# Kernel optimization log

Hardware: AMD Instinct MI355X
Metric: run time of the kernel (lower is better)

The kernel has to match this reference:

```python
import jax, jax.numpy as jnp
import numpy as np

N_NODES = 100000
N_EDGES = 1600000
N_GRAPHS = 128
ATOM_F = 92
BOND_F = 41
EMB = 64
HID = 128
CHG = 16
N_LAYERS = 3
EPS = 1e-5


def setup_inputs() -> dict:
    key = jax.random.key(0)
    ks = jax.random.split(key, 32)
    s = 0.05
    inp = {
        "x": jax.random.normal(ks[0], (N_NODES, ATOM_F), jnp.float32),
        "edge_attr": jax.random.uniform(ks[1], (N_EDGES, BOND_F), jnp.float32),
        "charge": jax.random.normal(ks[2], (N_GRAPHS,), jnp.float32),
        "edge_index": jax.random.randint(ks[3], (2, N_EDGES), 0, N_NODES),
        "batch": jnp.sort(jax.random.randint(ks[4], (N_NODES,), 0, N_GRAPHS)),
        # embeddings
        "W_charge": jax.random.normal(ks[5], (1, CHG), jnp.float32) * s,
        "b_charge": jnp.zeros((CHG,), jnp.float32),
        "W_atom": jax.random.normal(ks[6], (ATOM_F + CHG, EMB), jnp.float32) * s,
        "b_atom": jnp.zeros((EMB,), jnp.float32),
        "W_bond": jax.random.normal(ks[7], (BOND_F, EMB), jnp.float32) * s,
        "b_bond": jnp.zeros((EMB,), jnp.float32),
        # conv layers (stacked over layer dim)
        "conv_eW1": jax.random.normal(ks[8], (N_LAYERS, 3 * EMB, EMB), jnp.float32) * s,
        "conv_eb1": jnp.zeros((N_LAYERS, EMB), jnp.float32),
        "conv_eW2": jax.random.normal(ks[9], (N_LAYERS, EMB, EMB), jnp.float32) * s,
        "conv_eb2": jnp.zeros((N_LAYERS, EMB), jnp.float32),
        "conv_nW1": jax.random.normal(ks[10], (N_LAYERS, 2 * EMB, EMB), jnp.float32) * s,
        "conv_nb1": jnp.zeros((N_LAYERS, EMB), jnp.float32),
        "conv_nW2": jax.random.normal(ks[11], (N_LAYERS, EMB, EMB), jnp.float32) * s,
        "conv_nb2": jnp.zeros((N_LAYERS, EMB), jnp.float32),
        "bn_gamma": jnp.ones((N_LAYERS, EMB), jnp.float32),
        "bn_beta": jnp.zeros((N_LAYERS, EMB), jnp.float32),
        # predictor
        "pW1": jax.random.normal(ks[12], (EMB, HID), jnp.float32) * s,
        "pb1": jnp.zeros((HID,), jnp.float32),
        "pW2": jax.random.normal(ks[13], (HID, HID), jnp.float32) * s,
        "pb2": jnp.zeros((HID,), jnp.float32),
        "pW3": jax.random.normal(ks[14], (HID, 1), jnp.float32) * s,
        "pb3": jnp.zeros((1,), jnp.float32),
    }
    return inp


def reference(x, edge_attr, charge, W_charge, b_charge, W_atom, b_atom,
              W_bond, b_bond, conv_eW1, conv_eb1, conv_eW2, conv_eb2,
              conv_nW1, conv_nb1, conv_nW2, conv_nb2, bn_gamma, bn_beta,
              pW1, pb1, pW2, pb2, pW3, pb3, edge_index, batch):
    sp = jax.nn.softplus
    n_nodes = x.shape[0]
    n_graphs = charge.shape[0]

    # early charge integration: per-graph charge embedding broadcast to nodes
    charge_feat = charge[:, None] @ W_charge + b_charge          # [B, CHG]
    x = jnp.concatenate([x, charge_feat[batch]], axis=1)          # [N, ATOM_F+CHG]
    x = x @ W_atom + b_atom                                       # [N, EMB]
    ea = edge_attr @ W_bond + b_bond                              # [E, EMB]

    row, col = edge_index[0], edge_index[1]
    for i in range(conv_eW1.shape[0]):
        xr, xc = x[row], x[col]                                   # gathers [E, EMB]
        # edge update: MLP on [x_row, x_col, edge_attr]
        e_in = jnp.concatenate([xr, xc, ea], axis=1)              # [E, 3*EMB]
        ea = sp(e_in @ conv_eW1[i] + conv_eb1[i]) @ conv_eW2[i] + conv_eb2[i]
        # node messages: MLP on [x_row, new edge_attr]
        m_in = jnp.concatenate([xr, ea], axis=1)                  # [E, 2*EMB]
        msg = sp(m_in @ conv_nW1[i] + conv_nb1[i]) @ conv_nW2[i] + conv_nb2[i]
        x_new = jax.ops.segment_sum(msg, col, num_segments=n_nodes)
        # BatchNorm1d (training-mode batch stats, biased variance)
        mean = jnp.mean(x_new, axis=0)
        var = jnp.var(x_new, axis=0)
        x_new = (x_new - mean) * jax.lax.rsqrt(var + EPS) * bn_gamma[i] + bn_beta[i]
        x = sp(x_new) + x                                         # residual

    # global mean pool over graphs
    sums = jax.ops.segment_sum(x, batch, num_segments=n_graphs)   # [B, EMB]
    cnt = jax.ops.segment_sum(jnp.ones((n_nodes, 1), x.dtype), batch, num_segments=n_graphs)
    g = sums / jnp.maximum(cnt, 1.0)

    # predictor MLP (dropout is identity in eval mode)
    h = sp(g @ pW1 + pb1)
    h = sp(h @ pW2 + pb2)
    out = h @ pW3 + pb3                                           # [B, 1]
    return out.squeeze(-1)
```

## Files before the change

### kernel.cpp

```cpp
#include <hip/hip_runtime.h>
#include <math.h>

typedef short v8s __attribute__((ext_vector_type(8)));
typedef float v4f __attribute__((ext_vector_type(4)));
typedef unsigned int u32x4 __attribute__((ext_vector_type(4)));

__device__ __forceinline__ u32x4 nt_load4(const void* p) {
  return __builtin_nontemporal_load((const u32x4*)p);
}
__device__ __forceinline__ void nt_store4(void* p, u32x4 v) {
  __builtin_nontemporal_store(v, (u32x4*)p);
}

__device__ __forceinline__ float sp_f(float x) {
  return fmaxf(x, 0.0f) + 0.69314718056f * __log2f(1.0f + __expf(-fabsf(x)));
}

__device__ __forceinline__ unsigned short f2bf(float f) {
  union { float f; unsigned u; } x; x.f = f;
  unsigned r = (x.u + 0x7FFF + ((x.u >> 16) & 1)) >> 16;
  return (unsigned short)r;
}

__device__ __forceinline__ float bf2f(unsigned short h) {
  union { unsigned u; float f; } x; x.u = ((unsigned)h) << 16;
  return x.f;
}

__global__ __launch_bounds__(256) void k_prep_wfrag(
    const float* __restrict__ eW1, const float* __restrict__ eW2,
    const float* __restrict__ nW1, const float* __restrict__ nW2,
    const float* __restrict__ W_bond, unsigned short* __restrict__ wfrag) {
  if (blockIdx.x == 12) {
    unsigned short* out = wfrag + 12 * 4096;
    for (int f = threadIdx.x; f < 4096; f += 256) {
      int j = f & 7, ln = (f >> 3) & 63, kh = (f >> 9) & 1, ct = f >> 10;
      int k = kh * 32 + (ln >> 4) * 8 + j;
      int n = ct * 16 + (ln & 15);
      out[f] = (k < 41) ? f2bf(W_bond[k * 64 + n]) : 0;
    }
    return;
  }
  int i = blockIdx.x >> 2;
  int m = blockIdx.x & 3;
  const float* W;
  if (m == 0)      W = eW1 + (size_t)i * 192 * 64 + 128 * 64;
  else if (m == 1) W = eW2 + (size_t)i * 64 * 64;
  else if (m == 2) W = nW1 + (size_t)i * 128 * 64 + 64 * 64;
  else             W = nW2 + (size_t)i * 64 * 64;
  unsigned short* out = wfrag + ((size_t)i * 4 + m) * 4096;
  for (int f = threadIdx.x; f < 4096; f += 256) {
    int j = f & 7, ln = (f >> 3) & 63, kh = (f >> 9) & 1, ct = f >> 10;
    int k = kh * 32 + (ln >> 4) * 8 + j;
    int n = ct * 16 + (ln & 15);
    out[f] = f2bf(W[k * 64 + n]);
  }
}

__global__ __launch_bounds__(256) void k_embed_nodes(
    const float* __restrict__ x, const int* __restrict__ batch,
    const float* __restrict__ charge, const float* __restrict__ W_charge,
    const float* __restrict__ b_charge, const float* __restrict__ W_atom,
    const float* __restrict__ b_atom, float* __restrict__ xemb, int N) {
  __shared__ float sW[108 * 64];
  __shared__ float sX[128 * 92];
  __shared__ float sb[64];
  __shared__ float sWc[16];
  __shared__ float sbc[16];
  for (int i = threadIdx.x; i < 108 * 64; i += blockDim.x) sW[i] = W_atom[i];
  if (threadIdx.x < 64) sb[threadIdx.x] = b_atom[threadIdx.x];
  if (threadIdx.x < 16) {
    sWc[threadIdx.x] = W_charge[threadIdx.x];
    sbc[threadIdx.x] = b_charge[threadIdx.x];
  }
  int ntiles = (N + 127) >> 7;
  for (int tile = blockIdx.x; tile < ntiles; tile += gridDim.x) {
    int base = tile << 7;
    int cnt = N - base; if (cnt > 128) cnt = 128;
    __syncthreads();
    if (cnt == 128) {
      const u32x4* src = (const u32x4*)(x + (size_t)base * 92);
      for (int i = threadIdx.x; i < 2944; i += 256)
        ((u32x4*)sX)[i] = nt_load4(&src[i]);
    } else {
      for (int i = threadIdx.x; i < cnt * 92; i += 256)
        sX[i] = x[(size_t)base * 92 + i];
    }
    __syncthreads();
    int t = threadIdx.x;
    int node = t & 127, half = t >> 7;
    if (node < cnt) {
      int n = base + node;
      float acc[32];
#pragma unroll
      for (int j = 0; j < 32; ++j) acc[j] = sb[half * 32 + j];
      const float* xr = sX + node * 92;
      for (int k = 0; k < 92; ++k) {
        float a = xr[k];
        const float* wk = sW + k * 64 + half * 32;
#pragma unroll
        for (int j = 0; j < 32; ++j) acc[j] = fmaf(a, wk[j], acc[j]);
      }
      float ch = charge[batch[n]];
#pragma unroll
      for (int c = 0; c < 16; ++c) {
        float cf = fmaf(ch, sWc[c], sbc[c]);
        const float* wk = sW + (92 + c) * 64 + half * 32;
#pragma unroll
        for (int j = 0; j < 32; ++j) acc[j] = fmaf(cf, wk[j], acc[j]);
      }
      float* o = xemb + (size_t)n * 64 + half * 32;
#pragma unroll
      for (int q8 = 0; q8 < 8; ++q8)
        ((float4*)o)[q8] = make_float4(acc[4*q8], acc[4*q8+1], acc[4*q8+2], acc[4*q8+3]);
    }
  }
}

__global__ __launch_bounds__(256) void k_hist(const int* __restrict__ col,
                                              int* __restrict__ counts, int E) {
  int stride = gridDim.x * blockDim.x;
  for (int e = blockIdx.x * blockDim.x + threadIdx.x; e < E; e += stride)
    atomicAdd(&counts[col[e]], 1);
}

__global__ __launch_bounds__(256) void k_scan1(const int* __restrict__ counts,
                                               int* __restrict__ scan_tmp,
                                               int* __restrict__ bsum, int N) {
  __shared__ int sd[2][256];
  int t = threadIdx.x;
  int i = blockIdx.x * 256 + t;
  int v = (i < N) ? counts[i] : 0;
  sd[0][t] = v;
  __syncthreads();
  int s = 0;
#pragma unroll
  for (int off = 1; off < 256; off <<= 1) {
    int nv = sd[s][t];
    if (t >= off) nv += sd[s][t - off];
    sd[s ^ 1][t] = nv;
    s ^= 1;
    __syncthreads();
  }
  if (i < N) scan_tmp[i] = sd[s][t];
  if (t == 255) bsum[blockIdx.x] = sd[s][255];
}

__global__ __launch_bounds__(256) void k_scan2(int* __restrict__ b, int NB) {
  __shared__ int sd[2][256];
  __shared__ int carry_s;
  int t = threadIdx.x;
  if (t == 0) carry_s = 0;
  __syncthreads();
  for (int base = 0; base < NB; base += 256) {
    int i = base + t;
    int v = (i < NB) ? b[i] : 0;
    sd[0][t] = v;
    __syncthreads();
    int s = 0;
#pragma unroll
    for (int off = 1; off < 256; off <<= 1) {
      int nv = sd[s][t];
      if (t >= off) nv += sd[s][t - off];
      sd[s ^ 1][t] = nv;
      s ^= 1;
      __syncthreads();
    }
    int c = carry_s;
    int tot = sd[s][255];
    if (i < NB) b[i] = sd[s][t] + c;
    __syncthreads();
    if (t == 0) carry_s = c + tot;
    __syncthreads();
  }
}

__global__ __launch_bounds__(256) void k_scan3(const int* __restrict__ counts,
                                               const int* __restrict__ scan_tmp,
                                               const int* __restrict__ bsum,
                                               int* __restrict__ cursor, int N) {
  int i = blockIdx.x * 256 + threadIdx.x;
  if (i < N) {
    int base = (blockIdx.x > 0) ? bsum[blockIdx.x - 1] : 0;
    cursor[i] = scan_tmp[i] - counts[i] + base;
  }
}

__global__ __launch_bounds__(256) void k_scatter(
    const int* __restrict__ row, const int* __restrict__ col,
    int* __restrict__ cursor, int* __restrict__ pos,
    int* __restrict__ row_s, int* __restrict__ col_s, int E) {
  int stride = gridDim.x * blockDim.x;
  for (int e = blockIdx.x * blockDim.x + threadIdx.x; e < E; e += stride) {
    int c = col[e];
    int p = atomicAdd(&cursor[c], 1);
    pos[e] = p;
    row_s[p] = row[e];
    col_s[p] = c;
  }
}

__global__ __launch_bounds__(256) void k_embed_bonds_mfma(
    const float* __restrict__ eattr, const int* __restrict__ pos,
    const unsigned short* __restrict__ gWb, const float* __restrict__ b_bond,
    unsigned short* __restrict__ ea16, int E) {
  __shared__ unsigned short sA[128 * 64];
  __shared__ float sb[64];
  __shared__ int spos[128];
  int tid = threadIdx.x;
  int w = tid >> 6, l = tid & 63, q = l >> 4, c16 = l & 15;
  int rbase = w * 32;
  if (tid < 64) sb[tid] = b_bond[tid];
  int ntiles = (E + 127) >> 7;
  for (int tile = blockIdx.x; tile < ntiles; tile += gridDim.x) {
    int te = tile << 7;
    int cnt = E - te; if (cnt > 128) cnt = 128;
    __syncthreads();
    uint4 z = make_uint4(0, 0, 0, 0);
    for (int i = tid; i < 1024; i += 256) ((uint4*)sA)[i] = z;
    __syncthreads();
    int nflt = cnt * 41;
    for (int i = tid; i < nflt; i += 256) {
      int r = i / 41, k = i - r * 41;
      float v = __builtin_nontemporal_load(&eattr[(size_t)te * 41 + i]);
      sA[r * 64 + (k ^ ((r & 7) << 3))] = f2bf(v);
    }
    if (tid < 128) spos[tid] = (te + tid < E) ? pos[te + tid] : -1;
    __syncthreads();
    v8s bfr[4][2], af[2][2];
    v4f acc[2][4];
    const v8s* wp_ = (const v8s*)gWb;
#pragma unroll
    for (int ct = 0; ct < 4; ++ct)
#pragma unroll
      for (int kh = 0; kh < 2; ++kh)
        bfr[ct][kh] = wp_[(ct * 2 + kh) * 64 + l];
#pragma unroll
    for (int rb = 0; rb < 2; ++rb)
#pragma unroll
      for (int kh = 0; kh < 2; ++kh) {
        int row_ = rbase + rb * 16 + c16;
        af[rb][kh] = *(const v8s*)&sA[row_ * 64 +
                                      ((kh * 32 + q * 8) ^ ((row_ & 7) << 3))];
      }
#pragma unroll
    for (int rb = 0; rb < 2; ++rb)
#pragma unroll
      for (int ct = 0; ct < 4; ++ct) {
        v4f a_ = {0.f, 0.f, 0.f, 0.f};
        a_ = __builtin_amdgcn_mfma_f32_16x16x32_bf16(af[rb][0], bfr[ct][0], a_, 0, 0, 0);
        a_ = __builtin_amdgcn_mfma_f32_16x16x32_bf16(af[rb][1], bfr[ct][1], a_, 0, 0, 0);
        acc[rb][ct] = a_;
      }
#pragma unroll
    for (int rb = 0; rb < 2; ++rb)
#pragma unroll
      for (int ct = 0; ct < 4; ++ct) {
        int n = ct * 16 + c16;
#pragma unroll
        for (int r = 0; r < 4; ++r) {
          float v = acc[rb][ct][r] + sb[n];
          int row = rbase + rb * 16 + q * 4 + r;
          sA[row * 64 + (n ^ ((row & 7) << 3))] = f2bf(v);
        }
      }
    __syncthreads();
    for (int i = tid; i < 1024; i += 256) {
      int r = i >> 3, cc = i & 7;
      int p = spos[r];
      if (p >= 0) {
        u32x4 d = *(const u32x4*)&sA[r * 64 + ((cc * 8) ^ ((r & 7) << 3))];
        nt_store4(&ea16[(size_t)p * 64 + cc * 8], d);
      }
    }
  }
}

__device__ __forceinline__ void node_pre_body(
    const float* __restrict__ xr, const float* sWa, const float* sWb,
    const float* sWp, unsigned short* __restrict__ up16,
    unsigned short* __restrict__ v16, int n) {
  const float4* xr4 = (const float4*)xr;
  float u[64], p[64];
#pragma unroll
  for (int j = 0; j < 64; ++j) { u[j] = 0.f; p[j] = 0.f; }
  for (int k4 = 0; k4 < 16; ++k4) {
    float4 av = xr4[k4];
    const float* wa = sWa + k4 * 256;
    const float* wp = sWp + k4 * 256;
#pragma unroll
    for (int j = 0; j < 64; ++j) u[j] = fmaf(av.x, wa[j], u[j]);
#pragma unroll
    for (int j = 0; j < 64; ++j) p[j] = fmaf(av.x, wp[j], p[j]);
#pragma unroll
    for (int j = 0; j < 64; ++j) u[j] = fmaf(av.y, wa[64 + j], u[j]);
#pragma unroll
    for (int j = 0; j < 64; ++j) p[j] = fmaf(av.y, wp[64 + j], p[j]);
#pragma unroll
    for (int j = 0; j < 64; ++j) u[j] = fmaf(av.z, wa[128 + j], u[j]);
#pragma unroll
    for (int j = 0; j < 64; ++j) p[j] = fmaf(av.z, wp[128 + j], p[j]);
#pragma unroll
    for (int j = 0; j < 64; ++j) u[j] = fmaf(av.w, wa[192 + j], u[j]);
#pragma unroll
    for (int j = 0; j < 64; ++j) p[j] = fmaf(av.w, wp[192 + j], p[j]);
  }
  unsigned short* o = up16 + (size_t)n * 128;
#pragma unroll
  for (int q8 = 0; q8 < 8; ++q8) {
    unsigned short tmp[8];
#pragma unroll
    for (int j = 0; j < 8; ++j) {
      int i = q8 * 8 + j;
      tmp[j] = f2bf(u[((i & 3) << 4) | (i >> 2)]);
    }
    *(uint4*)&o[q8 * 8] = *(uint4*)tmp;
  }
#pragma unroll
  for (int q8 = 0; q8 < 8; ++q8) {
    unsigned short tmp[8];
#pragma unroll
    for (int j = 0; j < 8; ++j) {
      int i = q8 * 8 + j;
      tmp[j] = f2bf(p[((i & 3) << 4) | (i >> 2)]);
    }
    *(uint4*)&o[64 + q8 * 8] = *(uint4*)tmp;
  }
  float vv[64];
#pragma unroll
  for (int j = 0; j < 64; ++j) vv[j] = 0.f;
  for (int k4 = 0; k4 < 16; ++k4) {
    float4 av = xr4[k4];
    const float* wb = sWb + k4 * 256;
#pragma unroll
    for (int j = 0; j < 64; ++j) vv[j] = fmaf(av.x, wb[j], vv[j]);
#pragma unroll
    for (int j = 0; j < 64; ++j) vv[j] = fmaf(av.y, wb[64 + j], vv[j]);
#pragma unroll
    for (int j = 0; j < 64; ++j) vv[j] = fmaf(av.z, wb[128 + j], vv[j]);
#pragma unroll
    for (int j = 0; j < 64; ++j) vv[j] = fmaf(av.w, wb[192 + j], vv[j]);
  }
  unsigned short* ov = v16 + (size_t)n * 64;
#pragma unroll
  for (int q8 = 0; q8 < 8; ++q8) {
    unsigned short tmp[8];
#pragma unroll
    for (int j = 0; j < 8; ++j) {
      int i = q8 * 8 + j;
      tmp[j] = f2bf(vv[((i & 3) << 4) | (i >> 2)]);
    }
    *(uint4*)&ov[q8 * 8] = *(uint4*)tmp;
  }
}

__global__ __launch_bounds__(256) void k_node_pre(
    const float* __restrict__ xemb, const float* __restrict__ eW1,
    const float* __restrict__ nW1, unsigned short* __restrict__ up16,
    unsigned short* __restrict__ v16, float* __restrict__ xnew, int N) {
  __shared__ float sWa[64 * 64];
  __shared__ float sWb[64 * 64];
  __shared__ float sWp[64 * 64];
  for (int i = threadIdx.x; i < 64 * 64; i += blockDim.x) {
    sWa[i] = eW1[i];
    sWb[i] = eW1[64 * 64 + i];
    sWp[i] = nW1[i];
  }
  __syncthreads();
  int stride = gridDim.x * blockDim.x;
  float4 z = make_float4(0.f, 0.f, 0.f, 0.f);
  for (int n = blockIdx.x * blockDim.x + threadIdx.x; n < N; n += stride) {
    node_pre_body(xemb + (size_t)n * 64, sWa, sWb, sWp, up16, v16, n);
    float4* xz = (float4*)(xnew + (size_t)n * 64);
#pragma unroll
    for (int q = 0; q < 16; ++q) xz[q] = z;
  }
}

__global__ __launch_bounds__(256) void k_bn_pre(
    float* __restrict__ xemb, float* __restrict__ xnew,
    const float* __restrict__ bnacc, const float* __restrict__ gamma,
    const float* __restrict__ beta, const float* __restrict__ eW1n,
    const float* __restrict__ nW1n, unsigned short* __restrict__ up16,
    unsigned short* __restrict__ v16, int N) {
  __shared__ float sWa[64 * 64];
  __shared__ float sWb[64 * 64];
  __shared__ float sWp[64 * 64];
  __shared__ float sscale[64], sshift[64];
  for (int i = threadIdx.x; i < 64 * 64; i += blockDim.x) {
    sWa[i] = eW1n[i];
    sWb[i] = eW1n[64 * 64 + i];
    sWp[i] = nW1n[i];
  }
  if (threadIdx.x < 64) {
    float inv = 1.0f / (float)N;
    float m = bnacc[threadIdx.x] * inv;
    float var = bnacc[64 + threadIdx.x] * inv - m * m;
    float rs = rsqrtf(var + 1e-5f);
    float g = gamma[threadIdx.x];
    sscale[threadIdx.x] = rs * g;
    sshift[threadIdx.x] = beta[threadIdx.x] - m * rs * g;
  }
  __syncthreads();
  int stride = gridDim.x * blockDim.x;
  float4 z = make_float4(0.f, 0.f, 0.f, 0.f);
  for (int n = blockIdx.x * blockDim.x + threadIdx.x; n < N; n += stride) {
    float* xr = xemb + (size_t)n * 64;
    float4* xnrow = (float4*)(xnew + (size_t)n * 64);
#pragma unroll
    for (int q = 0; q < 16; ++q) {
      float4 xn4 = xnrow[q];
      float4 xo4 = ((const float4*)xr)[q];
      xo4.x += sp_f(fmaf(xn4.x, sscale[4*q+0], sshift[4*q+0]));
      xo4.y += sp_f(fmaf(xn4.y, sscale[4*q+1], sshift[4*q+1]));
      xo4.z += sp_f(fmaf(xn4.z, sscale[4*q+2], sshift[4*q+2]));
      xo4.w += sp_f(fmaf(xn4.w, sscale[4*q+3], sshift[4*q+3]));
      ((float4*)xr)[q] = xo4;
      xnrow[q] = z;
    }
    node_pre_body(xr, sWa, sWb, sWp, up16, v16, n);
  }
}

#define READ_FRAGS(P)                                                        \
  {                                                                          \
    const v8s* wp_ = (const v8s*)gWf + (P) * 512;                            \
    _Pragma("unroll") for (int ct = 0; ct < 4; ++ct)                         \
        _Pragma("unroll") for (int kh = 0; kh < 2; ++kh)                     \
            bfr[ct][kh] = wp_[(ct * 2 + kh) * 64 + l];                       \
    _Pragma("unroll") for (int rb = 0; rb < 2; ++rb)                         \
        _Pragma("unroll") for (int kh = 0; kh < 2; ++kh) {                   \
      int row_ = rbase + rb * 16 + c16;                                      \
      af[rb][kh] = *(const v8s*)&sA[row_ * 64 +                              \
                                    ((kh * 32 + q * 8) ^ ((row_ & 7) << 3))];\
    }                                                                        \
  }

#define DO_MFMA()                                                            \
  _Pragma("unroll") for (int rb = 0; rb < 2; ++rb)                           \
      _Pragma("unroll") for (int ct = 0; ct < 4; ++ct) {                     \
    v4f a_ = {0.f, 0.f, 0.f, 0.f};                                           \
    a_ = __builtin_amdgcn_mfma_f32_16x16x32_bf16(af[rb][0], bfr[ct][0], a_,  \
                                                 0, 0, 0);                   \
    a_ = __builtin_amdgcn_mfma_f32_16x16x32_bf16(af[rb][1], bfr[ct][1], a_,  \
                                                 0, 0, 0);                   \
    acc[rb][ct] = a_;                                                        \
  }

__global__ __launch_bounds__(256, 3) void k_edge_mfma(
    const int* __restrict__ row_s, const int* __restrict__ col_s,
    unsigned short* __restrict__ ea16, const unsigned short* __restrict__ up16,
    const unsigned short* __restrict__ v16,
    const unsigned short* __restrict__ gWf, const float* __restrict__ eb1,
    const float* __restrict__ eb2, const float* __restrict__ nb1,
    const float* __restrict__ nb2, float* __restrict__ xnew,
    float* __restrict__ bnacc, int E, int store_ea) {
  __shared__ __align__(16) unsigned char smem[41984];
  unsigned short* sA = (unsigned short*)smem;
  float* msgb        = (float*)smem;
  float* sBb         = (float*)(smem + 32768);
  int* scol          = (int*)(smem + 33792);

  int tid = threadIdx.x;
  int te = blockIdx.x * 128;
  int w = tid >> 6, l = tid & 63, q = l >> 4, c16 = l & 15;
  int rbase = w * 32;

  if (blockIdx.x == 0 && tid < 128) bnacc[tid] = 0.0f;

  int rid[2][4], cid[2][4], eid[2][4];
#pragma unroll
  for (int rb = 0; rb < 2; ++rb)
#pragma unroll
    for (int r = 0; r < 4; ++r) {
      int e = te + rbase + rb * 16 + q * 4 + r;
      eid[rb][r] = e;
      int ec = e < E ? e : E - 1;
      rid[rb][r] = row_s[ec];
      cid[rb][r] = col_s[ec];
    }
  ushort4 uu_pf[2][4], vv_pf[2][4];
#pragma unroll
  for (int rb = 0; rb < 2; ++rb)
#pragma unroll
    for (int r = 0; r < 4; ++r) {
      uu_pf[rb][r] = *(const ushort4*)&up16[(size_t)rid[rb][r] * 128 + c16 * 4];
      vv_pf[rb][r] = *(const ushort4*)&v16[(size_t)cid[rb][r] * 64 + c16 * 4];
    }

  if (tid < 64) {
    sBb[0 * 64 + tid] = eb1[tid];
    sBb[1 * 64 + tid] = eb2[tid];
    sBb[2 * 64 + tid] = nb1[tid];
    sBb[3 * 64 + tid] = nb2[tid];
  }
  if (tid < 128) {
    int e = te + tid;
    scol[tid] = col_s[e < E ? e : E - 1];
  }
  for (int i = tid; i < 1024; i += 256) {
    int r = i >> 3, cc = i & 7;
    int e = te + r;
    if (e >= E) e = E - 1;
    u32x4 d = nt_load4(&ea16[(size_t)e * 64 + cc * 8]);
    *(u32x4*)&sA[r * 64 + ((cc * 8) ^ ((r & 7) << 3))] = d;
  }

  v8s af[2][2];
  v8s bfr[4][2];
  v4f acc[2][4];

  __syncthreads();

  READ_FRAGS(0);
  DO_MFMA();
  ushort4 pp_pf[2][4];
#pragma unroll
  for (int rb = 0; rb < 2; ++rb)
#pragma unroll
    for (int r = 0; r < 4; ++r)
      pp_pf[rb][r] =
          *(const ushort4*)&up16[(size_t)rid[rb][r] * 128 + 64 + c16 * 4];
#pragma unroll
  for (int rb = 0; rb < 2; ++rb)
#pragma unroll
    for (int r = 0; r < 4; ++r) {
      const unsigned short* up_ = (const unsigned short*)&uu_pf[rb][r];
      const unsigned short* vp_ = (const unsigned short*)&vv_pf[rb][r];
      int row = rbase + rb * 16 + q * 4 + r;
#pragma unroll
      for (int ct = 0; ct < 4; ++ct) {
        int n = ct * 16 + c16;
        float t = acc[rb][ct][r] + sBb[n] + bf2f(up_[ct]) + bf2f(vp_[ct]);
        t = sp_f(t);
        sA[row * 64 + (n ^ ((row & 7) << 3))] = f2bf(t);
      }
    }

  READ_FRAGS(1);
  DO_MFMA();
#pragma unroll
  for (int rb = 0; rb < 2; ++rb)
#pragma unroll
    for (int ct = 0; ct < 4; ++ct) {
      int n = ct * 16 + c16;
#pragma unroll
      for (int r = 0; r < 4; ++r) {
        float en = acc[rb][ct][r] + sBb[64 + n];
        int row = rbase + rb * 16 + q * 4 + r;
        sA[row * 64 + (n ^ ((row & 7) << 3))] = f2bf(en);
      }
    }
  if (store_ea) {
    __syncthreads();
    for (int i = tid; i < 1024; i += 256) {
      int r = i >> 3, cc = i & 7;
      if (te + r < E) {
        u32x4 d = *(const u32x4*)&sA[r * 64 + ((cc * 8) ^ ((r & 7) << 3))];
        nt_store4(&ea16[(size_t)(te + r) * 64 + cc * 8], d);
      }
    }
    __syncthreads();
  }

  READ_FRAGS(2);
  DO_MFMA();
#pragma unroll
  for (int rb = 0; rb < 2; ++rb)
#pragma unroll
    for (int r = 0; r < 4; ++r) {
      const unsigned short* pp_ = (const unsigned short*)&pp_pf[rb][r];
      int row = rbase + rb * 16 + q * 4 + r;
#pragma unroll
      for (int ct = 0; ct < 4; ++ct) {
        int n = ct * 16 + c16;
        float t2 = acc[rb][ct][r] + sBb[128 + n] + bf2f(pp_[ct]);
        t2 = sp_f(t2);
        sA[row * 64 + (n ^ ((row & 7) << 3))] = f2bf(t2);
      }
    }

  READ_FRAGS(3);
  __syncthreads();
  DO_MFMA();
#pragma unroll
  for (int rb = 0; rb < 2; ++rb)
#pragma unroll
    for (int ct = 0; ct < 4; ++ct) {
      int n = ct * 16 + c16;
#pragma unroll
      for (int r = 0; r < 4; ++r) {
        float msg = acc[rb][ct][r] + sBb[192 + n];
        int row = rbase + rb * 16 + q * 4 + r;
        msgb[row * 64 + n] = (eid[rb][r] < E) ? msg : 0.0f;
      }
    }
  __syncthreads();

  int nrows = E - te;
  if (nrows > 128) nrows = 128;
  for (int r0 = w; r0 < nrows; r0 += 4) {
    int c0 = scol[r0];
    if (r0 > 0 && scol[r0 - 1] == c0) continue;
    float s = 0.0f;
    int r = r0;
    do {
      s += msgb[r * 64 + l];
      ++r;
    } while (r < nrows && scol[r] == c0);
    if (r0 > 0 && r < nrows)
      xnew[(size_t)c0 * 64 + l] = s;
    else
      atomicAdd(&xnew[(size_t)c0 * 64 + l], s);
  }
}

__global__ __launch_bounds__(256) void k_bn_stats(
    const float* __restrict__ xnew, float* __restrict__ bnacc, int N) {
  int t = threadIdx.x;
  int ch = t & 63;
  int sl = t >> 6;
  float s = 0.f, s2 = 0.f;
  for (int n = blockIdx.x * 4 + sl; n < N; n += gridDim.x * 4) {
    float v = xnew[(size_t)n * 64 + ch];
    s += v;
    s2 = fmaf(v, v, s2);
  }
  __shared__ float red[256], red2[256];
  red[t] = s;
  red2[t] = s2;
  __syncthreads();
  if (sl == 0) {
    s = red[ch] + red[64 + ch] + red[128 + ch] + red[192 + ch];
    s2 = red2[ch] + red2[64 + ch] + red2[128 + ch] + red2[192 + ch];
    atomicAdd(&bnacc[ch], s);
    atomicAdd(&bnacc[64 + ch], s2);
  }
}

__global__ __launch_bounds__(256) void k_bn_apply(
    float* __restrict__ x, const float* __restrict__ xnew,
    const float* __restrict__ bnacc, const float* __restrict__ gamma,
    const float* __restrict__ beta, int N) {
  __shared__ float sscale[64], sshift[64];
  if (threadIdx.x < 64) {
    float inv = 1.0f / (float)N;
    float m = bnacc[threadIdx.x] * inv;
    float var = bnacc[64 + threadIdx.x] * inv - m * m;
    float rs = rsqrtf(var + 1e-5f);
    float g = gamma[threadIdx.x];
    sscale[threadIdx.x] = rs * g;
    sshift[threadIdx.x] = beta[threadIdx.x] - m * rs * g;
  }
  __syncthreads();
  size_t total = (size_t)N * 64;
  size_t stride = (size_t)gridDim.x * blockDim.x;
  for (size_t i = (size_t)blockIdx.x * blockDim.x + threadIdx.x; i < total; i += stride) {
    int ch = (int)(i & 63);
    float v = fmaf(xnew[i], sscale[ch], sshift[ch]);
    x[i] += sp_f(v);
  }
}

__device__ __forceinline__ int lbound(const int* a, int n, int key) {
  int lo = 0, hi = n;
  while (lo < hi) {
    int mid = (lo + hi) >> 1;
    if (a[mid] < key) lo = mid + 1; else hi = mid;
  }
  return lo;
}

__global__ __launch_bounds__(256) void k_pool_pred(
    const float* __restrict__ x, const int* __restrict__ batch, int N,
    const float* __restrict__ pW1, const float* __restrict__ pb1,
    const float* __restrict__ pW2, const float* __restrict__ pb2,
    const float* __restrict__ pW3, const float* __restrict__ pb3,
    float* __restrict__ out) {
  int b = blockIdx.x;
  int lo = lbound(batch, N, b);
  int hi = lbound(batch, N, b + 1);
  int t = threadIdx.x;
  int ch = t & 63;
  int sl = t >> 6;
  float s = 0.f;
  for (int n = lo + sl; n < hi; n += 4) s += x[(size_t)n * 64 + ch];
  __shared__ float red4[4][64];
  __shared__ float sg[64];
  __shared__ float sh1[128];
  __shared__ float red[128];
  red4[sl][ch] = s;
  __syncthreads();
  if (t < 64) {
    float tot = red4[0][t] + red4[1][t] + red4[2][t] + red4[3][t];
    float cnt = (float)(hi - lo);
    sg[t] = tot / fmaxf(cnt, 1.0f);
  }
  __syncthreads();
  if (t < 128) {
    float h = pb1[t];
    for (int k = 0; k < 64; ++k) h = fmaf(sg[k], pW1[k * 128 + t], h);
    sh1[t] = sp_f(h);
  }
  __syncthreads();
  if (t < 128) {
    float h = pb2[t];
    for (int k = 0; k < 128; ++k) h = fmaf(sh1[k], pW2[k * 128 + t], h);
    red[t] = sp_f(h) * pW3[t];
  }
  __syncthreads();
  for (int off = 64; off > 0; off >>= 1) {
    if (t < off) red[t] += red[t + off];
    __syncthreads();
  }
  if (t == 0) out[b] = red[0] + pb3[0];
}

extern "C" void kernel_launch(void* const* d_in, const int* in_sizes, int n_in,
                              void* d_out, int out_size, void* d_ws, size_t ws_size,
                              hipStream_t stream) {
  const float* x         = (const float*)d_in[0];
  const float* edge_attr = (const float*)d_in[1];
  const float* charge    = (const float*)d_in[2];
  const int*   eidx      = (const int*)d_in[3];
  const int*   batch     = (const int*)d_in[4];
  const float* W_charge  = (const float*)d_in[5];
  const float* b_charge  = (const float*)d_in[6];
  const float* W_atom    = (const float*)d_in[7];
  const float* b_atom    = (const float*)d_in[8];
  const float* W_bond    = (const float*)d_in[9];
  const float* b_bond    = (const float*)d_in[10];
  const float* eW1 = (const float*)d_in[11];
  const float* eb1 = (const float*)d_in[12];
  const float* eW2 = (const float*)d_in[13];
  const float* eb2 = (const float*)d_in[14];
  const float* nW1 = (const float*)d_in[15];
  const float* nb1 = (const float*)d_in[16];
  const float* nW2 = (const float*)d_in[17];
  const float* nb2 = (const float*)d_in[18];
  const float* gam = (const float*)d_in[19];
  const float* bet = (const float*)d_in[20];
  const float* pW1 = (const float*)d_in[21];
  const float* pb1 = (const float*)d_in[22];
  const float* pW2 = (const float*)d_in[23];
  const float* pb2 = (const float*)d_in[24];
  const float* pW3 = (const float*)d_in[25];
  const float* pb3 = (const float*)d_in[26];

  int N = in_sizes[4];
  int E = in_sizes[3] / 2;
  int B = in_sizes[2];
  const int* row = eidx;
  const int* col = eidx + E;

  char* wptr = (char*)d_ws;
  unsigned short* ea16 = (unsigned short*)wptr; wptr += (((size_t)E * 64 * 2 + 255) & ~255ull);
  unsigned short* up16 = (unsigned short*)wptr; wptr += (((size_t)N * 128 * 2 + 255) & ~255ull);
  unsigned short* v16  = (unsigned short*)wptr; wptr += (((size_t)N * 64 * 2 + 255) & ~255ull);
  unsigned short* wfrag = (unsigned short*)wptr; wptr += 13 * 4096 * 2;
  float* xemb = (float*)wptr; wptr += (size_t)N * 64 * 4;
  float* xnew = (float*)wptr; wptr += (size_t)N * 64 * 4;
  float* bnacc = (float*)wptr; wptr += 256 * 4;
  int* counts = (int*)wptr;   wptr += (size_t)N * 4;
  int* scan_tmp = (int*)wptr; wptr += (size_t)N * 4;
  int* cursor = (int*)wptr;   wptr += (size_t)N * 4;
  int* bsum = (int*)wptr;     wptr += 4096;
  int* pos = (int*)wptr;      wptr += (size_t)E * 4;
  int* row_s = (int*)wptr;    wptr += (size_t)E * 4;
  int* col_s = (int*)wptr;    wptr += (size_t)E * 4;

  int NB = (N + 255) / 256;

  k_prep_wfrag<<<13, 256, 0, stream>>>(eW1, eW2, nW1, nW2, W_bond, wfrag);
  hipMemsetAsync(counts, 0, (size_t)N * 4, stream);
  k_hist<<<2048, 256, 0, stream>>>(col, counts, E);
  k_scan1<<<NB, 256, 0, stream>>>(counts, scan_tmp, bsum, N);
  k_scan2<<<1, 256, 0, stream>>>(bsum, NB);
  k_scan3<<<NB, 256, 0, stream>>>(counts, scan_tmp, bsum, cursor, N);
  k_scatter<<<2048, 256, 0, stream>>>(row, col, cursor, pos, row_s, col_s, E);

  int ntilesN = (N + 127) / 128;
  k_embed_nodes<<<ntilesN, 256, 0, stream>>>(x, batch, charge, W_charge,
                                             b_charge, W_atom, b_atom, xemb, N);
  k_embed_bonds_mfma<<<2048, 256, 0, stream>>>(edge_attr, pos,
                                               wfrag + 12 * 4096, b_bond,
                                               ea16, E);
  k_node_pre<<<NB, 256, 0, stream>>>(xemb, eW1, nW1, up16, v16, xnew, N);

  int gridE = (E + 127) / 128;
  for (int i = 0; i < 3; ++i) {
    k_edge_mfma<<<gridE, 256, 0, stream>>>(
        row_s, col_s, ea16, up16, v16, wfrag + (size_t)i * 16384,
        eb1 + (size_t)i * 64, eb2 + (size_t)i * 64, nb1 + (size_t)i * 64,
        nb2 + (size_t)i * 64, xnew, bnacc, E, (i < 2) ? 1 : 0);
    k_bn_stats<<<1024, 256, 0, stream>>>(xnew, bnacc, N);
    if (i < 2) {
      k_bn_pre<<<NB, 256, 0, stream>>>(
          xemb, xnew, bnacc, gam + (size_t)i * 64, bet + (size_t)i * 64,
          eW1 + (size_t)(i + 1) * 192 * 64, nW1 + (size_t)(i + 1) * 128 * 64,
          up16, v16, N);
    } else {
      k_bn_apply<<<4096, 256, 0, stream>>>(xemb, xnew, bnacc,
                                           gam + (size_t)i * 64,
                                           bet + (size_t)i * 64, N);
    }
  }

  k_pool_pred<<<B, 256, 0, stream>>>(xemb, batch, N, pW1, pb1, pW2, pb2,
                                     pW3, pb3, (float*)d_out);
}
```

Before: 2.002 ms.

## Split edge MFMA tile across 8 waves with 16 rows each

The edge kernel now launches 512 threads per 128-edge tile instead of 256, so each wave handles one 16-row MFMA block instead of two. Per-thread fragment, accumulator and prefetch arrays are halved, which lowers register pressure; the launch bounds are raised to 512 threads with 6 blocks per CU. The aim is more resident waves to hide the latency of the gathered up16/v16 loads and the global traffic. In exchange, every wave reloads the full weight fragments, so weight reads per edge double, and block-wide synchronisation now spans more waves.

```diff
diff --git a/kernel.cpp b/kernel.cpp
--- a/kernel.cpp
+++ b/kernel.cpp
@@ -428,26 +428,25 @@
     _Pragma("unroll") for (int ct = 0; ct < 4; ++ct)                         \
         _Pragma("unroll") for (int kh = 0; kh < 2; ++kh)                     \
             bfr[ct][kh] = wp_[(ct * 2 + kh) * 64 + l];                       \
-    _Pragma("unroll") for (int rb = 0; rb < 2; ++rb)                         \
-        _Pragma("unroll") for (int kh = 0; kh < 2; ++kh) {                   \
-      int row_ = rbase + rb * 16 + c16;                                      \
-      af[rb][kh] = *(const v8s*)&sA[row_ * 64 +                              \
-                                    ((kh * 32 + q * 8) ^ ((row_ & 7) << 3))];\
+    {                                                                        \
+      int row_ = rbase + c16;                                                \
+      _Pragma("unroll") for (int kh = 0; kh < 2; ++kh)                       \
+        af[kh] = *(const v8s*)&sA[row_ * 64 +                                \
+                                  ((kh * 32 + q * 8) ^ ((row_ & 7) << 3))];  \
     }                                                                        \
   }
 
 #define DO_MFMA()                                                            \
-  _Pragma("unroll") for (int rb = 0; rb < 2; ++rb)                           \
-      _Pragma("unroll") for (int ct = 0; ct < 4; ++ct) {                     \
+  _Pragma("unroll") for (int ct = 0; ct < 4; ++ct) {                         \
     v4f a_ = {0.f, 0.f, 0.f, 0.f};                                           \
-    a_ = __builtin_amdgcn_mfma_f32_16x16x32_bf16(af[rb][0], bfr[ct][0], a_,  \
+    a_ = __builtin_amdgcn_mfma_f32_16x16x32_bf16(af[0], bfr[ct][0], a_,      \
                                                  0, 0, 0);                   \
-    a_ = __builtin_amdgcn_mfma_f32_16x16x32_bf16(af[rb][1], bfr[ct][1], a_,  \
+    a_ = __builtin_amdgcn_mfma_f32_16x16x32_bf16(af[1], bfr[ct][1], a_,      \
                                                  0, 0, 0);                   \
-    acc[rb][ct] = a_;                                                        \
-  }
-
-__global__ __launch_bounds__(256, 3) void k_edge_mfma(
+    acc[ct] = a_;                                                            \
+  }
+
+__global__ __launch_bounds__(512, 6) void k_edge_mfma(
     const int* __restrict__ row_s, const int* __restrict__ col_s,
     unsigned short* __restrict__ ea16, const unsigned short* __restrict__ up16,
     const unsigned short* __restrict__ v16,
@@ -464,29 +463,25 @@
   int tid = threadIdx.x;
   int te = blockIdx.x * 128;
   int w = tid >> 6, l = tid & 63, q = l >> 4, c16 = l & 15;
-  int rbase = w * 32;
+  int rbase = w * 16;
 
   if (blockIdx.x == 0 && tid < 128) bnacc[tid] = 0.0f;
 
-  int rid[2][4], cid[2][4], eid[2][4];
-#pragma unroll
-  for (int rb = 0; rb < 2; ++rb)
-#pragma unroll
-    for (int r = 0; r < 4; ++r) {
-      int e = te + rbase + rb * 16 + q * 4 + r;
-      eid[rb][r] = e;
-      int ec = e < E ? e : E - 1;
-      rid[rb][r] = row_s[ec];
-      cid[rb][r] = col_s[ec];
-    }
-  ushort4 uu_pf[2][4], vv_pf[2][4];
-#pragma unroll
-  for (int rb = 0; rb < 2; ++rb)
-#pragma unroll
-    for (int r = 0; r < 4; ++r) {
-      uu_pf[rb][r] = *(const ushort4*)&up16[(size_t)rid[rb][r] * 128 + c16 * 4];
-      vv_pf[rb][r] = *(const ushort4*)&v16[(size_t)cid[rb][r] * 64 + c16 * 4];
-    }
+  int rid[4], cid[4], eid[4];
+#pragma unroll
+  for (int r = 0; r < 4; ++r) {
+    int e = te + rbase + q * 4 + r;
+    eid[r] = e;
+    int ec = e < E ? e : E - 1;
+    rid[r] = row_s[ec];
+    cid[r] = col_s[ec];
+  }
+  ushort4 uu_pf[4], vv_pf[4];
+#pragma unroll
+  for (int r = 0; r < 4; ++r) {
+    uu_pf[r] = *(const ushort4*)&up16[(size_t)rid[r] * 128 + c16 * 4];
+    vv_pf[r] = *(const ushort4*)&v16[(size_t)cid[r] * 64 + c16 * 4];
+  }
 
   if (tid < 64) {
     sBb[0 * 64 + tid] = eb1[tid];
@@ -498,7 +493,7 @@
     int e = te + tid;
     scol[tid] = col_s[e < E ? e : E - 1];
   }
-  for (int i = tid; i < 1024; i += 256) {
+  for (int i = tid; i < 1024; i += 512) {
     int r = i >> 3, cc = i & 7;
     int e = te + r;
     if (e >= E) e = E - 1;
@@ -506,54 +501,47 @@
     *(u32x4*)&sA[r * 64 + ((cc * 8) ^ ((r & 7) << 3))] = d;
   }
 
-  v8s af[2][2];
+  v8s af[2];
   v8s bfr[4][2];
-  v4f acc[2][4];
+  v4f acc[4];
 
   __syncthreads();
 
   READ_FRAGS(0);
   DO_MFMA();
-  ushort4 pp_pf[2][4];
-#pragma unroll
-  for (int rb = 0; rb < 2; ++rb)
-#pragma unroll
-    for (int r = 0; r < 4; ++r)
-      pp_pf[rb][r] =
-          *(const ushort4*)&up16[(size_t)rid[rb][r] * 128 + 64 + c16 * 4];
-#pragma unroll
-  for (int rb = 0; rb < 2; ++rb)
-#pragma unroll
-    for (int r = 0; r < 4; ++r) {
-      const unsigned short* up_ = (const unsigned short*)&uu_pf[rb][r];
-      const unsigned short* vp_ = (const unsigned short*)&vv_pf[rb][r];
-      int row = rbase + rb * 16 + q * 4 + r;
-#pragma unroll
-      for (int ct = 0; ct < 4; ++ct) {
-        int n = ct * 16 + c16;
-        float t = acc[rb][ct][r] + sBb[n] + bf2f(up_[ct]) + bf2f(vp_[ct]);
-        t = sp_f(t);
-        sA[row * 64 + (n ^ ((row & 7) << 3))] = f2bf(t);
-      }
-    }
+  ushort4 pp_pf[4];
+#pragma unroll
+  for (int r = 0; r < 4; ++r)
+    pp_pf[r] = *(const ushort4*)&up16[(size_t)rid[r] * 128 + 64 + c16 * 4];
+#pragma unroll
+  for (int r = 0; r < 4; ++r) {
+    const unsigned short* up_ = (const unsigned short*)&uu_pf[r];
+    const unsigned short* vp_ = (const unsigned short*)&vv_pf[r];
+    int row = rbase + q * 4 + r;
+#pragma unroll
+    for (int ct = 0; ct < 4; ++ct) {
+      int n = ct * 16 + c16;
+      float t = acc[ct][r] + sBb[n] + bf2f(up_[ct]) + bf2f(vp_[ct]);
+      t = sp_f(t);
+      sA[row * 64 + (n ^ ((row & 7) << 3))] = f2bf(t);
+    }
+  }
 
   READ_FRAGS(1);
   DO_MFMA();
 #pragma unroll
-  for (int rb = 0; rb < 2; ++rb)
-#pragma unroll
-    for (int ct = 0; ct < 4; ++ct) {
-      int n = ct * 16 + c16;
-#pragma unroll
-      for (int r = 0; r < 4; ++r) {
-        float en = acc[rb][ct][r] + sBb[64 + n];
-        int row = rbase + rb * 16 + q * 4 + r;
-        sA[row * 64 + (n ^ ((row & 7) << 3))] = f2bf(en);
-      }
-    }
+  for (int ct = 0; ct < 4; ++ct) {
+    int n = ct * 16 + c16;
+#pragma unroll
+    for (int r = 0; r < 4; ++r) {
+      float en = acc[ct][r] + sBb[64 + n];
+      int row = rbase + q * 4 + r;
+      sA[row * 64 + (n ^ ((row & 7) << 3))] = f2bf(en);
+    }
+  }
   if (store_ea) {
     __syncthreads();
-    for (int i = tid; i < 1024; i += 256) {
+    for (int i = tid; i < 1024; i += 512) {
       int r = i >> 3, cc = i & 7;
       if (te + r < E) {
         u32x4 d = *(const u32x4*)&sA[r * 64 + ((cc * 8) ^ ((r & 7) << 3))];
@@ -566,40 +554,36 @@
   READ_FRAGS(2);
   DO_MFMA();
 #pragma unroll
-  for (int rb = 0; rb < 2; ++rb)
-#pragma unroll
-    for (int r = 0; r < 4; ++r) {
-      const unsigned short* pp_ = (const unsigned short*)&pp_pf[rb][r];
-      int row = rbase + rb * 16 + q * 4 + r;
-#pragma unroll
-      for (int ct = 0; ct < 4; ++ct) {
-        int n = ct * 16 + c16;
-        float t2 = acc[rb][ct][r] + sBb[128 + n] + bf2f(pp_[ct]);
-        t2 = sp_f(t2);
-        sA[row * 64 + (n ^ ((row & 7) << 3))] = f2bf(t2);
-      }
-    }
-
-  READ_FRAGS(3);
-  __syncthreads();
-  DO_MFMA();
-#pragma unroll
-  for (int rb = 0; rb < 2; ++rb)
+  for (int r = 0; r < 4; ++r) {
+    const unsigned short* pp_ = (const unsigned short*)&pp_pf[r];
+    int row = rbase + q * 4 + r;
 #pragma unroll
     for (int ct = 0; ct < 4; ++ct) {
       int n = ct * 16 + c16;
-#pragma unroll
-      for (int r = 0; r < 4; ++r) {
-        float msg = acc[rb][ct][r] + sBb[192 + n];
-        int row = rbase + rb * 16 + q * 4 + r;
-        msgb[row * 64 + n] = (eid[rb][r] < E) ? msg : 0.0f;
-      }
-    }
+      float t2 = acc[ct][r] + sBb[128 + n] + bf2f(pp_[ct]);
+      t2 = sp_f(t2);
+      sA[row * 64 + (n ^ ((row & 7) << 3))] = f2bf(t2);
+    }
+  }
+
+  READ_FRAGS(3);
+  __syncthreads();
+  DO_MFMA();
+#pragma unroll
+  for (int ct = 0; ct < 4; ++ct) {
+    int n = ct * 16 + c16;
+#pragma unroll
+    for (int r = 0; r < 4; ++r) {
+      float msg = acc[ct][r] + sBb[192 + n];
+      int row = rbase + q * 4 + r;
+      msgb[row * 64 + n] = (eid[r] < E) ? msg : 0.0f;
+    }
+  }
   __syncthreads();
 
   int nrows = E - te;
   if (nrows > 128) nrows = 128;
-  for (int r0 = w; r0 < nrows; r0 += 4) {
+  for (int r0 = w; r0 < nrows; r0 += 8) {
     int c0 = scol[r0];
     if (r0 > 0 && scol[r0 - 1] == c0) continue;
     float s = 0.0f;
@@ -789,7 +773,7 @@
 
   int gridE = (E + 127) / 128;
   for (int i = 0; i < 3; ++i) {
-    k_edge_mfma<<<gridE, 256, 0, stream>>>(
+    k_edge_mfma<<<gridE, 512, 0, stream>>>(
         row_s, col_s, ea16, up16, v16, wfrag + (size_t)i * 16384,
         eb1 + (size_t)i * 64, eb2 + (size_t)i * 64, nb1 + (size_t)i * 64,
         nb2 + (size_t)i * 64, xnew, bnacc, E, (i < 2) ? 1 : 0);
```

After: 1.993 ms (median of 2 runs). No clear change (-0.5%).
